# Optimization experiments

Measured on AMD Instinct MI355X. Metric: run time of the kernel, lower is better.

## Reference

```python
import jax, jax.numpy as jnp
import numpy as np

R = 16
LORA_ALPHA = 32
SCALING = LORA_ALPHA / R  # use_rslora=False -> alpha/r = 2.0


def fwht(x):
    """Normalized fast Walsh-Hadamard transform along last axis (power-of-2 dim)."""
    n = x.shape[-1]
    batch = x.shape[:-1]
    h = 1
    while h < n:  # static loop, log2(n) iterations
        x = x.reshape(*batch, n // (2 * h), 2, h)
        a = x[..., 0, :]
        b = x[..., 1, :]
        x = jnp.stack([a + b, a - b], axis=-2).reshape(*batch, n)
        h *= 2
    return x * np.float32(1.0 / np.sqrt(n))


def quant_int8_ste(x):
    """Simulated symmetric per-row int8 quantization with straight-through estimator."""
    s = jnp.max(jnp.abs(x), axis=-1, keepdims=True) * np.float32(1.0 / 127.0)
    s = jnp.maximum(s, np.float32(1e-8))
    q = jnp.clip(jnp.round(x / s), -127.0, 127.0) * s
    return x + jax.lax.stop_gradient(q - x)


def setup_inputs() -> dict:
    key = jax.random.key(0)
    k1, k2, k3, k4 = jax.random.split(key, 4)
    B, S, D_in, D_out = 4, 2048, 4096, 4096
    x = jax.random.normal(k1, (B, S, D_in), dtype=jnp.float32)
    weight = jax.random.normal(k2, (D_out, D_in), dtype=jnp.float32) * np.float32(0.02)
    lora_A = jax.random.normal(k3, (R, D_in), dtype=jnp.float32) * np.float32(0.02)
    lora_B = jax.random.normal(k4, (D_out, R), dtype=jnp.float32) * np.float32(0.02)
    return {"x": x, "weight": weight, "lora_A": lora_A, "lora_B": lora_B}


def reference(x, weight, lora_A, lora_B):
    B, S, D_in = x.shape
    x2 = x.reshape(-1, D_in)  # [B*S, D_in]
    # Hadamard-rotate + quantize both operands (rotation is orthogonal, so
    # (xH)(WH)^T == xW^T up to quantization error) then GEMM.
    xq = quant_int8_ste(fwht(x2))          # [B*S, D_in]
    wq = quant_int8_ste(fwht(weight))      # [D_out, D_in]
    out = xq @ wq.T                        # [B*S, D_out]
    # LoRA side path (dropout p=0): B(A x) * scaling
    lora = (x2 @ lora_A.T) @ lora_B.T * np.float32(SCALING)
    return (out + lora).reshape(B, S, -1)
```

## Files before the change

### kernel.cpp

```cpp
#include <hip/hip_runtime.h>
#include <stdint.h>

typedef int v4i __attribute__((ext_vector_type(4)));
typedef int v16i __attribute__((ext_vector_type(16)));

#define GLD_LDS16(gp, lp)                                                              \
  __builtin_amdgcn_global_load_lds((const __attribute__((address_space(1))) void*)(gp), \
                                   (__attribute__((address_space(3))) void*)(lp), 16, 0, 0)

__device__ __forceinline__ v4i lds_read_b128(uint32_t off) {
  v4i r;
  asm volatile("ds_read_b128 %0, %1" : "=v"(r) : "v"(off));
  return r;
}

__device__ __forceinline__ void fwht16(float v[16]) {
#pragma unroll
  for (int h = 1; h < 16; h <<= 1) {
#pragma unroll
    for (int i = 0; i < 16; ++i) {
      if (!(i & h)) {
        float a = v[i], b = v[i | h];
        v[i] = a + b;
        v[i | h] = a - b;
      }
    }
  }
}

__device__ __forceinline__ void fwht_row_load(const float* __restrict__ xr, int t,
                                              float v[16]) {
  const float4* p = reinterpret_cast<const float4*>(xr) + t * 4;
  float4 a = p[0], b = p[1], c = p[2], d = p[3];
  v[0] = a.x; v[1] = a.y; v[2] = a.z; v[3] = a.w;
  v[4] = b.x; v[5] = b.y; v[6] = b.z; v[7] = b.w;
  v[8] = c.x; v[9] = c.y; v[10] = c.z; v[11] = c.w;
  v[12] = d.x; v[13] = d.y; v[14] = d.z; v[15] = d.w;
}

__device__ __forceinline__ void fwht4096(float v[16], float* lds, int t) {
  fwht16(v);
#pragma unroll
  for (int e = 0; e < 16; ++e) {
    int idx = t * 16 + e;
    lds[idx + (idx >> 5)] = v[e];
  }
  __syncthreads();
#pragma unroll
  for (int e = 0; e < 16; ++e) {
    int idx = ((t >> 4) << 8) + (e << 4) + (t & 15);
    v[e] = lds[idx + (idx >> 5)];
  }
  fwht16(v);
#pragma unroll
  for (int e = 0; e < 16; ++e) {
    int idx = ((t >> 4) << 8) + (e << 4) + (t & 15);
    lds[idx + (idx >> 5)] = v[e];
  }
  __syncthreads();
#pragma unroll
  for (int e = 0; e < 16; ++e) {
    int idx = (e << 8) + t;
    v[e] = lds[idx + (idx >> 5)];
  }
  fwht16(v);
#pragma unroll
  for (int e = 0; e < 16; ++e) v[e] *= 0.015625f;
}

__global__ __launch_bounds__(256) void fwht_quant_kernel(const float* __restrict__ X,
                                                         int8_t* __restrict__ Q,
                                                         float* __restrict__ S) {
  const int row = blockIdx.x;
  const int t = threadIdx.x;
  __shared__ float lds[4224];
  __shared__ float wred[4];

  float v[16];
  fwht_row_load(X + (size_t)row * 4096, t, v);
  fwht4096(v, lds, t);

  float m = 0.f;
#pragma unroll
  for (int e = 0; e < 16; ++e) m = fmaxf(m, fabsf(v[e]));
#pragma unroll
  for (int off = 32; off > 0; off >>= 1) m = fmaxf(m, __shfl_xor(m, off));
  if ((t & 63) == 0) wred[t >> 6] = m;
  __syncthreads();
  m = fmaxf(fmaxf(wred[0], wred[1]), fmaxf(wred[2], wred[3]));
  const float s = fmaxf(m * (1.0f / 127.0f), 1e-8f);
  if (t == 0) S[row] = s;
  int8_t* qr = Q + (size_t)row * 4096;
#pragma unroll
  for (int e = 0; e < 16; ++e) {
    float q = rintf(v[e] / s);
    q = fminf(fmaxf(q, -127.f), 127.f);
    qr[(e << 8) + t] = (int8_t)(int)q;
  }
}

__global__ __launch_bounds__(256) void fwht_nq_kernel(const float* __restrict__ X,
                                                      float* __restrict__ F) {
  const int row = blockIdx.x;
  const int t = threadIdx.x;
  __shared__ float lds[4224];
  float v[16];
  fwht_row_load(X + (size_t)row * 4096, t, v);
  fwht4096(v, lds, t);
  float* fr = F + (size_t)row * 4096;
#pragma unroll
  for (int e = 0; e < 16; ++e) fr[(e << 8) + t] = v[e];
}

__global__ __launch_bounds__(256) void lora_t_partial_q(const int8_t* __restrict__ Qx,
                                                        const float* __restrict__ Sx,
                                                        const float* __restrict__ Ah,
                                                        float* __restrict__ tpart) {
  __shared__ float As[16][512];
  const int t = threadIdx.x;
  const int kc = blockIdx.y;
  const int row = blockIdx.x * 256 + t;
  for (int i = t; i < 2048; i += 256) {
    int r = i >> 7, c4 = i & 127;
    reinterpret_cast<float4*>(&As[r][0])[c4] =
        reinterpret_cast<const float4*>(Ah + (size_t)r * 4096 + kc * 512)[c4];
  }
  __syncthreads();
  float acc[16];
#pragma unroll
  for (int r = 0; r < 16; ++r) acc[r] = 0.f;
  const int8_t* xr = Qx + (size_t)row * 4096 + kc * 512;
  for (int k = 0; k < 512; k += 16) {
    int4 pv = *reinterpret_cast<const int4*>(xr + k);
    int us[4] = {pv.x, pv.y, pv.z, pv.w};
#pragma unroll
    for (int b = 0; b < 4; ++b) {
#pragma unroll
      for (int j = 0; j < 4; ++j) {
        float f = (float)((int)(int8_t)(us[b] >> (8 * j)));
        int kk = k + b * 4 + j;
#pragma unroll
        for (int r = 0; r < 16; ++r) acc[r] = fmaf(f, As[r][kk], acc[r]);
      }
    }
  }
  const float s = Sx[row];
  float* tp = tpart + ((size_t)kc * 8192 + row) * 16;
#pragma unroll
  for (int r = 0; r < 16; ++r) tp[r] = acc[r] * s;
}

__global__ __launch_bounds__(256) void lora_t_reduce_kernel(const float* __restrict__ tpart,
                                                            float* __restrict__ tmat) {
  int i = blockIdx.x * 256 + threadIdx.x;
  float s = 0.f;
#pragma unroll
  for (int kc = 0; kc < 8; ++kc) s += tpart[(size_t)kc * 131072 + i];
  tmat[i] = s;
}

__global__ __launch_bounds__(512, 4) void gemm_i8_kernel(
    const int8_t* __restrict__ Aq, const int8_t* __restrict__ Bq,
    const float* __restrict__ Sx, const float* __restrict__ Sw,
    const float* __restrict__ Tm, const float* __restrict__ LB,
    float* __restrict__ out) {
  __shared__ __align__(16) char smem[73728];

  const int tid = threadIdx.x;
  const int lane = tid & 63;
  const int w = tid >> 6;
  const int wm = w >> 1;
  const int wn = w & 1;

  int bid = (int)blockIdx.x;
  bid = (bid & 7) * 128 + (bid >> 3);
  const int bm = bid >> 5;
  const int bn = bid & 31;

  const int8_t* Ag = Aq + (size_t)bm * 256 * 4096;
  const int8_t* Bg = Bq + (size_t)bn * 128 * 4096;

  const uint32_t sbase = (uint32_t)(uintptr_t)(void*)smem;

  const uint32_t srcOff = (uint32_t)(((lane & 3) ^ ((lane >> 3) & 3)) << 4);
  const uint32_t gA0 = (uint32_t)((w * 32 + (lane >> 2)) * 4096) + srcOff;
  const uint32_t gA1 = gA0 + 16 * 4096;
  const uint32_t gB0 = (uint32_t)((w * 16 + (lane >> 2)) * 4096) + srcOff;

#define STAGE_STEP(s, bufbase)                                           \
  do {                                                                   \
    const uint32_t kb = (uint32_t)(s) << 6;                              \
    GLD_LDS16(Ag + kb + gA0, smem + (bufbase) + w * 2048);               \
    GLD_LDS16(Ag + kb + gA1, smem + (bufbase) + w * 2048 + 1024);        \
    GLD_LDS16(Bg + kb + gB0, smem + (bufbase) + 16384 + w * 1024);       \
  } while (0)

  int aoff[2][2], boff[2][2];
  const int swz = (lane >> 1) & 3;
  const int khalf = lane >> 5;
#pragma unroll
  for (int mt = 0; mt < 2; ++mt) {
    int r = wm * 64 + mt * 32 + (lane & 31);
#pragma unroll
    for (int ks = 0; ks < 2; ++ks) {
      int c = ((ks << 1) | khalf) ^ swz;
      aoff[mt][ks] = r * 64 + (c << 4);
    }
  }
#pragma unroll
  for (int nt = 0; nt < 2; ++nt) {
    int r = wn * 64 + nt * 32 + (lane & 31);
#pragma unroll
    for (int ks = 0; ks < 2; ++ks) {
      int c = ((ks << 1) | khalf) ^ swz;
      boff[nt][ks] = 16384 + r * 64 + (c << 4);
    }
  }

  v16i acc[2][2];
#pragma unroll
  for (int i = 0; i < 2; ++i)
#pragma unroll
    for (int n = 0; n < 2; ++n) {
      v16i z = {0};
      acc[i][n] = z;
    }

  STAGE_STEP(0, 0);
  STAGE_STEP(1, 24576);
  asm volatile("s_waitcnt vmcnt(3)" ::: "memory");
  __builtin_amdgcn_s_barrier();
  __builtin_amdgcn_sched_barrier(0);

  uint32_t bc = 0, bn1 = 24576, bn2 = 49152;

#pragma unroll 1
  for (int t = 0; t < 64; ++t) {
    if (t <= 61) STAGE_STEP(t + 2, bn2);

    const uint32_t R = sbase + bc;
    v4i a0[2], b0[2], a1[2], b1[2];
    b0[0] = lds_read_b128(R + boff[0][0]);
    b0[1] = lds_read_b128(R + boff[1][0]);
    a0[0] = lds_read_b128(R + aoff[0][0]);
    a0[1] = lds_read_b128(R + aoff[1][0]);
    b1[0] = lds_read_b128(R + boff[0][1]);
    b1[1] = lds_read_b128(R + boff[1][1]);
    a1[0] = lds_read_b128(R + aoff[0][1]);
    a1[1] = lds_read_b128(R + aoff[1][1]);

    asm volatile("s_waitcnt lgkmcnt(4)" ::: "memory");
    __builtin_amdgcn_sched_barrier(0);
    __builtin_amdgcn_s_setprio(1);
    acc[0][0] = __builtin_amdgcn_mfma_i32_32x32x32_i8(a0[0], b0[0], acc[0][0], 0, 0, 0);
    acc[0][1] = __builtin_amdgcn_mfma_i32_32x32x32_i8(a0[0], b0[1], acc[0][1], 0, 0, 0);
    acc[1][0] = __builtin_amdgcn_mfma_i32_32x32x32_i8(a0[1], b0[0], acc[1][0], 0, 0, 0);
    acc[1][1] = __builtin_amdgcn_mfma_i32_32x32x32_i8(a0[1], b0[1], acc[1][1], 0, 0, 0);
    __builtin_amdgcn_s_setprio(0);

    asm volatile("s_waitcnt lgkmcnt(0)" ::: "memory");
    __builtin_amdgcn_sched_barrier(0);
    __builtin_amdgcn_s_setprio(1);
    acc[0][0] = __builtin_amdgcn_mfma_i32_32x32x32_i8(a1[0], b1[0], acc[0][0], 0, 0, 0);
    acc[0][1] = __builtin_amdgcn_mfma_i32_32x32x32_i8(a1[0], b1[1], acc[0][1], 0, 0, 0);
    acc[1][0] = __builtin_amdgcn_mfma_i32_32x32x32_i8(a1[1], b1[0], acc[1][0], 0, 0, 0);
    acc[1][1] = __builtin_amdgcn_mfma_i32_32x32x32_i8(a1[1], b1[1], acc[1][1], 0, 0, 0);
    __builtin_amdgcn_s_setprio(0);

    if (t <= 61)
      asm volatile("s_waitcnt vmcnt(3)" ::: "memory");
    else if (t == 62)
      asm volatile("s_waitcnt vmcnt(0)" ::: "memory");
    __builtin_amdgcn_s_barrier();
    __builtin_amdgcn_sched_barrier(0);

    uint32_t tmp = bc;
    bc = bn1;
    bn1 = bn2;
    bn2 = tmp;
  }

  __syncthreads();
  float* tl = (float*)smem;
  float* bl = (float*)(smem + 17408);
  for (int i = tid; i < 1024; i += 512) {
    int r = i >> 2, q4 = (i & 3) * 4;
    float4 tv = *reinterpret_cast<const float4*>(Tm + (size_t)(bm * 256 + r) * 16 + q4);
    tl[r * 17 + q4 + 0] = tv.x;
    tl[r * 17 + q4 + 1] = tv.y;
    tl[r * 17 + q4 + 2] = tv.z;
    tl[r * 17 + q4 + 3] = tv.w;
  }
  for (int i = tid; i < 512; i += 512) {
    int r = i >> 2, q4 = (i & 3) * 4;
    float4 bv = *reinterpret_cast<const float4*>(LB + (size_t)(bn * 128 + r) * 16 + q4);
    bl[r * 17 + q4 + 0] = bv.x;
    bl[r * 17 + q4 + 1] = bv.y;
    bl[r * 17 + q4 + 2] = bv.z;
    bl[r * 17 + q4 + 3] = bv.w;
  }
  __syncthreads();

  float blv[2][16], swv[2];
#pragma unroll
  for (int nt = 0; nt < 2; ++nt) {
    int cl = wn * 64 + nt * 32 + (lane & 31);
    swv[nt] = Sw[bn * 128 + cl];
#pragma unroll
    for (int q = 0; q < 16; ++q) blv[nt][q] = bl[cl * 17 + q];
  }
#pragma unroll
  for (int mt = 0; mt < 2; ++mt) {
#pragma unroll
    for (int rg = 0; rg < 16; ++rg) {
      int rl = wm * 64 + mt * 32 + (rg & 3) + 8 * (rg >> 2) + 4 * (lane >> 5);
      float sxv = Sx[bm * 256 + rl];
      float tv[16];
#pragma unroll
      for (int q = 0; q < 16; ++q) tv[q] = tl[rl * 17 + q];
      float* orow = out + (size_t)(bm * 256 + rl) * 4096 + bn * 128;
#pragma unroll
      for (int nt = 0; nt < 2; ++nt) {
        float dot = 0.f;
#pragma unroll
        for (int q = 0; q < 16; ++q) dot = fmaf(tv[q], blv[nt][q], dot);
        int cl = wn * 64 + nt * 32 + (lane & 31);
        orow[cl] = sxv * swv[nt] * (float)acc[mt][nt][rg] + 2.0f * dot;
      }
    }
  }
}

extern "C" void kernel_launch(void* const* d_in, const int* in_sizes, int n_in,
                              void* d_out, int out_size, void* d_ws, size_t ws_size,
                              hipStream_t stream) {
  const float* x = (const float*)d_in[0];
  const float* wgt = (const float*)d_in[1];
  const float* lA = (const float*)d_in[2];
  const float* lB = (const float*)d_in[3];
  float* out = (float*)d_out;

  char* ws = (char*)d_ws;
  int8_t* qx = (int8_t*)ws;
  int8_t* qw = (int8_t*)(ws + 33554432);
  float* sx = (float*)(ws + 50331648);
  float* sw = (float*)(ws + 50364416);
  float* tmat = (float*)(ws + 50380800);
  float* tpart = (float*)(ws + 50905088);
  float* Ah = (float*)(ws + 55099392);

  fwht_quant_kernel<<<8192, 256, 0, stream>>>(x, qx, sx);
  fwht_quant_kernel<<<4096, 256, 0, stream>>>(wgt, qw, sw);
  fwht_nq_kernel<<<16, 256, 0, stream>>>(lA, Ah);
  lora_t_partial_q<<<dim3(32, 8), 256, 0, stream>>>(qx, sx, Ah, tpart);
  lora_t_reduce_kernel<<<512, 256, 0, stream>>>(tpart, tmat);
  gemm_i8_kernel<<<1024, 512, 0, stream>>>(qx, qw, sx, sw, tmat, lB, out);
}
```

Baseline: 299.3 us.

## Prefetch next-stage LDS fragments across barrier and pack int8 quant stores

```diff
diff --git a/kernel.cpp b/kernel.cpp
--- a/kernel.cpp
+++ b/kernel.cpp
@@ -73,7 +73,7 @@
                                                          float* __restrict__ S) {
   const int row = blockIdx.x;
   const int t = threadIdx.x;
-  __shared__ float lds[4224];
+  __shared__ __align__(16) float lds[4224];
   __shared__ float wred[4];
 
   float v[16];
@@ -90,20 +90,26 @@
   m = fmaxf(fmaxf(wred[0], wred[1]), fmaxf(wred[2], wred[3]));
   const float s = fmaxf(m * (1.0f / 127.0f), 1e-8f);
   if (t == 0) S[row] = s;
-  int8_t* qr = Q + (size_t)row * 4096;
+
+  __syncthreads();
+  char* b8 = (char*)lds;
 #pragma unroll
   for (int e = 0; e < 16; ++e) {
     float q = rintf(v[e] / s);
     q = fminf(fmaxf(q, -127.f), 127.f);
-    qr[(e << 8) + t] = (int8_t)(int)q;
-  }
+    int idx = (e << 8) + t;
+    b8[idx + ((idx >> 8) << 4)] = (char)(int)q;
+  }
+  __syncthreads();
+  int4 pack = *reinterpret_cast<const int4*>(b8 + t * 16 + ((t >> 4) << 4));
+  reinterpret_cast<int4*>(Q + (size_t)row * 4096)[t] = pack;
 }
 
 __global__ __launch_bounds__(256) void fwht_nq_kernel(const float* __restrict__ X,
                                                       float* __restrict__ F) {
   const int row = blockIdx.x;
   const int t = threadIdx.x;
-  __shared__ float lds[4224];
+  __shared__ __align__(16) float lds[4224];
   float v[16];
   fwht_row_load(X + (size_t)row * 4096, t, v);
   fwht4096(v, lds, t);
@@ -159,7 +165,7 @@
   tmat[i] = s;
 }
 
-__global__ __launch_bounds__(512, 4) void gemm_i8_kernel(
+__global__ __launch_bounds__(512, 2) void gemm_i8_kernel(
     const int8_t* __restrict__ Aq, const int8_t* __restrict__ Bq,
     const float* __restrict__ Sx, const float* __restrict__ Sw,
     const float* __restrict__ Tm, const float* __restrict__ LB,
@@ -232,6 +238,14 @@
   __builtin_amdgcn_s_barrier();
   __builtin_amdgcn_sched_barrier(0);
 
+  v4i a0c[2], b0c[2];
+  b0c[0] = lds_read_b128(sbase + boff[0][0]);
+  b0c[1] = lds_read_b128(sbase + boff[1][0]);
+  a0c[0] = lds_read_b128(sbase + aoff[0][0]);
+  a0c[1] = lds_read_b128(sbase + aoff[1][0]);
+  asm volatile("s_waitcnt lgkmcnt(0)" ::: "memory");
+  __builtin_amdgcn_sched_barrier(0);
+
   uint32_t bc = 0, bn1 = 24576, bn2 = 49152;
 
 #pragma unroll 1
@@ -239,40 +253,46 @@
     if (t <= 61) STAGE_STEP(t + 2, bn2);
 
     const uint32_t R = sbase + bc;
-    v4i a0[2], b0[2], a1[2], b1[2];
-    b0[0] = lds_read_b128(R + boff[0][0]);
-    b0[1] = lds_read_b128(R + boff[1][0]);
-    a0[0] = lds_read_b128(R + aoff[0][0]);
-    a0[1] = lds_read_b128(R + aoff[1][0]);
+    v4i a1[2], b1[2];
     b1[0] = lds_read_b128(R + boff[0][1]);
     b1[1] = lds_read_b128(R + boff[1][1]);
     a1[0] = lds_read_b128(R + aoff[0][1]);
     a1[1] = lds_read_b128(R + aoff[1][1]);
 
-    asm volatile("s_waitcnt lgkmcnt(4)" ::: "memory");
-    __builtin_amdgcn_sched_barrier(0);
     __builtin_amdgcn_s_setprio(1);
-    acc[0][0] = __builtin_amdgcn_mfma_i32_32x32x32_i8(a0[0], b0[0], acc[0][0], 0, 0, 0);
-    acc[0][1] = __builtin_amdgcn_mfma_i32_32x32x32_i8(a0[0], b0[1], acc[0][1], 0, 0, 0);
-    acc[1][0] = __builtin_amdgcn_mfma_i32_32x32x32_i8(a0[1], b0[0], acc[1][0], 0, 0, 0);
-    acc[1][1] = __builtin_amdgcn_mfma_i32_32x32x32_i8(a0[1], b0[1], acc[1][1], 0, 0, 0);
+    acc[0][0] = __builtin_amdgcn_mfma_i32_32x32x32_i8(a0c[0], b0c[0], acc[0][0], 0, 0, 0);
+    acc[0][1] = __builtin_amdgcn_mfma_i32_32x32x32_i8(a0c[0], b0c[1], acc[0][1], 0, 0, 0);
+    acc[1][0] = __builtin_amdgcn_mfma_i32_32x32x32_i8(a0c[1], b0c[0], acc[1][0], 0, 0, 0);
+    acc[1][1] = __builtin_amdgcn_mfma_i32_32x32x32_i8(a0c[1], b0c[1], acc[1][1], 0, 0, 0);
     __builtin_amdgcn_s_setprio(0);
-
     asm volatile("s_waitcnt lgkmcnt(0)" ::: "memory");
     __builtin_amdgcn_sched_barrier(0);
+
+    if (t <= 61)
+      asm volatile("s_waitcnt vmcnt(3)" ::: "memory");
+    else if (t == 62)
+      asm volatile("s_waitcnt vmcnt(0)" ::: "memory");
+    __builtin_amdgcn_sched_barrier(0);
+    __builtin_amdgcn_s_barrier();
+
+    if (t < 63) {
+      const uint32_t Rn = sbase + bn1;
+      b0c[0] = lds_read_b128(Rn + boff[0][0]);
+      b0c[1] = lds_read_b128(Rn + boff[1][0]);
+      a0c[0] = lds_read_b128(Rn + aoff[0][0]);
+      a0c[1] = lds_read_b128(Rn + aoff[1][0]);
+    }
+
     __builtin_amdgcn_s_setprio(1);
     acc[0][0] = __builtin_amdgcn_mfma_i32_32x32x32_i8(a1[0], b1[0], acc[0][0], 0, 0, 0);
     acc[0][1] = __builtin_amdgcn_mfma_i32_32x32x32_i8(a1[0], b1[1], acc[0][1], 0, 0, 0);
     acc[1][0] = __builtin_amdgcn_mfma_i32_32x32x32_i8(a1[1], b1[0], acc[1][0], 0, 0, 0);
     acc[1][1] = __builtin_amdgcn_mfma_i32_32x32x32_i8(a1[1], b1[1], acc[1][1], 0, 0, 0);
     __builtin_amdgcn_s_setprio(0);
-
-    if (t <= 61)
-      asm volatile("s_waitcnt vmcnt(3)" ::: "memory");
-    else if (t == 62)
-      asm volatile("s_waitcnt vmcnt(0)" ::: "memory");
-    __builtin_amdgcn_s_barrier();
-    __builtin_amdgcn_sched_barrier(0);
+    if (t < 63) {
+      asm volatile("s_waitcnt lgkmcnt(0)" ::: "memory");
+      __builtin_amdgcn_sched_barrier(0);
+    }
 
     uint32_t tmp = bc;
     bc = bn1;
```

After: 294.7 us. No clear change (-1.5%).
